# Kernel tuning notes

Measured on AMD Instinct MI355X. Metric: run time of the kernel, lower is better.

## Reference

```python
import jax, jax.numpy as jnp
import numpy as np

N_NODES = 100000


def gcn_conv(x, edge_index, edge_weight, W, b):
    """PyG GCNConv: out = D^-1/2 (A + I) D^-1/2 X W + b (self-loop weight 1)."""
    n = x.shape[0]
    src, dst = edge_index[0], edge_index[1]
    loop = jnp.arange(n)
    src_sl = jnp.concatenate([src, loop])
    dst_sl = jnp.concatenate([dst, loop])
    ew_sl = jnp.concatenate([edge_weight, jnp.ones((n,), x.dtype)])
    deg = jax.ops.segment_sum(ew_sl, dst_sl, num_segments=n)  # [N]
    dinv = jnp.where(deg > 0, jax.lax.rsqrt(deg), 0.0)
    norm = dinv[src_sl] * ew_sl * dinv[dst_sl]  # [E+N]
    h = x @ W  # [N, out_dim] dense transform before propagation
    msg = h[src_sl] * norm[:, None]  # gather + scale, [E+N, out_dim]
    out = jax.ops.segment_sum(msg, dst_sl, num_segments=n)  # scatter-add
    return out + b


def setup_inputs() -> dict:
    key = jax.random.key(0)
    ks = jax.random.split(key, 9)
    in_dim, hidden, latent = 128, 64, 32
    n, e = N_NODES, 1600000
    x = jax.random.normal(ks[0], (n, in_dim), dtype=jnp.float32)
    edge_index = jax.random.randint(ks[1], (2, e), 0, n, dtype=jnp.int64)
    edge_weight = jax.random.uniform(ks[2], (e,), dtype=jnp.float32)
    def glorot(k, fan_in, fan_out):
        s = jnp.sqrt(6.0 / (fan_in + fan_out))
        return jax.random.uniform(k, (fan_in, fan_out), jnp.float32, -s, s)
    return {
        "x": x,
        "edge_index": edge_index,
        "edge_weight": edge_weight,
        "W1": glorot(ks[3], in_dim, hidden),
        "b1": jnp.zeros((hidden,), jnp.float32),
        "W_mu": glorot(ks[4], hidden, latent),
        "b_mu": jnp.zeros((latent,), jnp.float32),
        "W_lv": glorot(ks[5], hidden, latent),
        "b_lv": jnp.zeros((latent,), jnp.float32),
    }


def reference(x, edge_index, edge_weight, W1, b1, W_mu, b_mu, W_lv, b_lv):
    h = jax.nn.relu(gcn_conv(x, edge_index, edge_weight, W1, b1))
    mu = gcn_conv(h, edge_index, edge_weight, W_mu, b_mu)
    logvar = gcn_conv(h, edge_index, edge_weight, W_lv, b_lv)
    return (mu, logvar)
```

## Files before the change

### kernel.cpp

```cpp
#include <hip/hip_runtime.h>

static __device__ __forceinline__ float4 ld4(const float* p) { return *(const float4*)p; }
static __device__ __forceinline__ float b2f(unsigned short u) {
    return __uint_as_float((unsigned)u << 16);
}
static __device__ __forceinline__ float b2f_lo(unsigned u) { return __uint_as_float(u << 16); }
static __device__ __forceinline__ float b2f_hi(unsigned u) { return __uint_as_float(u & 0xFFFF0000u); }
static __device__ __forceinline__ unsigned short f2b(float f) {
    unsigned x = __float_as_uint(f);
    return (unsigned short)((x + 0x7FFFu + ((x >> 16) & 1u)) >> 16);
}

#define NPB 512


__global__ __launch_bounds__(1024) void k_bin(const int* __restrict__ src,
                                              const int* __restrict__ dst,
                                              const float* __restrict__ ew,
                                              int* __restrict__ bin_cnt,
                                              unsigned long long* __restrict__ ebuf,
                                              int E, int capE, int NB) {
    extern __shared__ int sh[];
    int* h = sh;
    int* base = sh + NB;
    int tid = threadIdx.x;
    for (int j = tid; j < NB; j += 1024) h[j] = 0;
    __syncthreads();
    int e0 = blockIdx.x * 4096;
    unsigned long long pk[4]; int b[4], loc[4]; bool act[4];
    #pragma unroll
    for (int i = 0; i < 4; i++) {
        int e = e0 + i * 1024 + tid;
        act[i] = e < E;
        if (act[i]) {
            int s = src[e];
            int d = dst[e];
            float w = ew[e];
            b[i] = d >> 9;
            pk[i] = ((unsigned long long)__float_as_uint(w) << 32) |
                    (unsigned)((d & (NPB - 1)) << 17) | (unsigned)s;
            loc[i] = atomicAdd(&h[b[i]], 1);
        }
    }
    __syncthreads();
    for (int j = tid; j < NB; j += 1024) base[j] = atomicAdd(&bin_cnt[j], h[j]);
    __syncthreads();
    #pragma unroll
    for (int i = 0; i < 4; i++) {
        if (act[i]) ebuf[(size_t)b[i] * capE + base[b[i]] + loc[i]] = pk[i];
    }
}

__global__ __launch_bounds__(512) void k_csr_build(const unsigned long long* __restrict__ ebuf,
                                                   const int* __restrict__ bin_cnt,
                                                   int2* __restrict__ rowcnt,
                                                   float* __restrict__ dinv,
                                                   unsigned long long* __restrict__ csr,
                                                   int n, int capE) {
    __shared__ unsigned cntL[NPB];
    __shared__ unsigned ewsL[NPB];
    __shared__ int scanL[NPB];
    __shared__ int rowL[NPB];
    __shared__ unsigned fillL[NPB];
    __shared__ int binbase_s;
    int b = blockIdx.x;
    int tid = threadIdx.x;
    cntL[tid] = 0; ewsL[tid] = 0; fillL[tid] = 0;
    scanL[tid] = (tid < b) ? bin_cnt[tid] : 0;
    __syncthreads();
    int m = bin_cnt[b];
    const unsigned long long* eb = ebuf + (size_t)b * capE;
    for (int i = tid; i < m; i += 512) {
        unsigned long long pk = eb[i];
        int ld = (int)((pk >> 17) & (NPB - 1));
        float w = __uint_as_float((unsigned)(pk >> 32));
        atomicAdd(&cntL[ld], 1u);
        atomicAdd(&ewsL[ld], (unsigned)(w * 16777216.0f));
    }
    __syncthreads();
    #pragma unroll
    for (int off = 256; off > 0; off >>= 1) {
        if (tid < off) scanL[tid] += scanL[tid + off];
        __syncthreads();
    }
    if (tid == 0) binbase_s = scanL[0];
    __syncthreads();
    int v = (int)cntL[tid];
    scanL[tid] = v;
    __syncthreads();
    #pragma unroll
    for (int off = 1; off < 512; off <<= 1) {
        int t = (tid >= off) ? scanL[tid - off] : 0;
        __syncthreads();
        scanL[tid] += t;
        __syncthreads();
    }
    int rp = binbase_s + scanL[tid] - v;
    rowL[tid] = rp;
    int node = b * NPB + tid;
    if (node < n) {
        rowcnt[node] = make_int2(rp, v);
        dinv[node] = rsqrtf(1.0f + (float)ewsL[tid] * (1.0f / 16777216.0f));
    }
    __syncthreads();
    for (int i = tid; i < m; i += 512) {
        unsigned long long pk = eb[i];
        int s = (int)(pk & 0x1FFFF);
        int ld = (int)((pk >> 17) & (NPB - 1));
        int pos = rowL[ld] + (int)atomicAdd(&fillL[ld], 1u);
        csr[pos] = (unsigned long long)(unsigned)s | (pk & 0xFFFFFFFF00000000ull);
    }
}

template<int K, bool SPLITW, bool ABF16>
__global__ __launch_bounds__(256) void k_gemm(const void* __restrict__ Av,
                                              const float* __restrict__ W0,
                                              const float* __restrict__ W1s,
                                              const float* __restrict__ dinv,
                                              unsigned short* __restrict__ out, int n) {
    __shared__ float Ws[K * 64];
    __shared__ float Xs[64 * K];
    int tid = threadIdx.x;
    int row0 = blockIdx.x * 64;

    constexpr int WF4 = K * 64 / 4;
    for (int j = tid; j < WF4; j += 256) {
        float4 v;
        if (!SPLITW) {
            v = ld4(W0 + j * 4);
        } else {
            int k = (j * 4) >> 6;
            int c = (j * 4) & 63;
            v = (c < 32) ? ld4(W0 + k * 32 + c) : ld4(W1s + k * 32 + (c - 32));
        }
        *(float4*)&Ws[j * 4] = v;
    }
    constexpr int XF4PR = K / 4;
    for (int j = tid; j < 64 * XF4PR; j += 256) {
        int r = j / XF4PR, kc = j % XF4PR;
        int grow = row0 + r;
        float4 v = make_float4(0.f, 0.f, 0.f, 0.f);
        if (grow < n) {
            if (ABF16) {
                const unsigned short* Ab = (const unsigned short*)Av;
                ushort4 u = *(const ushort4*)(Ab + (size_t)grow * K + kc * 4);
                v = make_float4(b2f(u.x), b2f(u.y), b2f(u.z), b2f(u.w));
            } else {
                v = ld4((const float*)Av + (size_t)grow * K + kc * 4);
            }
        }
        *(float4*)&Xs[r * K + kc * 4] = v;
    }
    __syncthreads();

    int c0 = (tid & 15) * 4;
    int r0 = (tid >> 4) * 4;
    float4 acc[4] = {};
    #pragma unroll 4
    for (int kk = 0; kk < K; kk += 4) {
        float4 w0 = ld4(&Ws[(kk + 0) * 64 + c0]);
        float4 w1 = ld4(&Ws[(kk + 1) * 64 + c0]);
        float4 w2 = ld4(&Ws[(kk + 2) * 64 + c0]);
        float4 w3 = ld4(&Ws[(kk + 3) * 64 + c0]);
        #pragma unroll
        for (int i = 0; i < 4; i++) {
            float4 a = ld4(&Xs[(r0 + i) * K + kk]);
            acc[i].x = fmaf(a.x, w0.x, fmaf(a.y, w1.x, fmaf(a.z, w2.x, fmaf(a.w, w3.x, acc[i].x))));
            acc[i].y = fmaf(a.x, w0.y, fmaf(a.y, w1.y, fmaf(a.z, w2.y, fmaf(a.w, w3.y, acc[i].y))));
            acc[i].z = fmaf(a.x, w0.z, fmaf(a.y, w1.z, fmaf(a.z, w2.z, fmaf(a.w, w3.z, acc[i].z))));
            acc[i].w = fmaf(a.x, w0.w, fmaf(a.y, w1.w, fmaf(a.z, w2.w, fmaf(a.w, w3.w, acc[i].w))));
        }
    }
    #pragma unroll
    for (int i = 0; i < 4; i++) {
        int grow = row0 + r0 + i;
        if (grow < n) {
            float sc = dinv[grow];
            ushort4 u = make_ushort4(f2b(acc[i].x * sc), f2b(acc[i].y * sc),
                                     f2b(acc[i].z * sc), f2b(acc[i].w * sc));
            *(ushort4*)&out[(size_t)grow * 64 + c0] = u;
        }
    }
}

template<bool RELU, bool SPLIT_OUT>
__global__ __launch_bounds__(256) void k_prop(const unsigned short* __restrict__ g,
                                              const int2* __restrict__ csr,
                                              const int2* __restrict__ rowcnt,
                                              const float* __restrict__ dinv,
                                              const float* __restrict__ bias0,
                                              const float* __restrict__ bias1,
                                              void* __restrict__ outv, int n) {
    int node = blockIdx.x * 4 + (threadIdx.x >> 6);
    if (node >= n) return;
    int lane = threadIdx.x & 63;
    int q = lane >> 4;
    int t = lane & 15;
    float a0 = 0.f, a1 = 0.f, a2 = 0.f, a3 = 0.f;
    int2 rc = rowcnt[node];
    const int2* ep = csr + rc.x;
    int m = rc.y;
    for (int e = 0; e < m; e += 8) {
        int e1 = e + q, e2 = e + 4 + q;
        if (e1 < m) {
            int2 p = ep[e1];
            uint2 r = *(const uint2*)(g + (size_t)p.x * 64 + t * 4);
            float nm = __int_as_float(p.y);
            a0 = fmaf(b2f_lo(r.x), nm, a0);
            a1 = fmaf(b2f_hi(r.x), nm, a1);
            a2 = fmaf(b2f_lo(r.y), nm, a2);
            a3 = fmaf(b2f_hi(r.y), nm, a3);
        }
        if (e2 < m) {
            int2 p = ep[e2];
            uint2 r = *(const uint2*)(g + (size_t)p.x * 64 + t * 4);
            float nm = __int_as_float(p.y);
            a0 = fmaf(b2f_lo(r.x), nm, a0);
            a1 = fmaf(b2f_hi(r.x), nm, a1);
            a2 = fmaf(b2f_lo(r.y), nm, a2);
            a3 = fmaf(b2f_hi(r.y), nm, a3);
        }
    }
    a0 += __shfl_xor(a0, 16); a0 += __shfl_xor(a0, 32);
    a1 += __shfl_xor(a1, 16); a1 += __shfl_xor(a1, 32);
    a2 += __shfl_xor(a2, 16); a2 += __shfl_xor(a2, 32);
    a3 += __shfl_xor(a3, 16); a3 += __shfl_xor(a3, 32);
    if (q != 0) return;
    uint2 sr = *(const uint2*)(g + (size_t)node * 64 + t * 4);
    a0 += b2f_lo(sr.x); a1 += b2f_hi(sr.x);
    a2 += b2f_lo(sr.y); a3 += b2f_hi(sr.y);
    float di = dinv[node];
    a0 *= di; a1 *= di; a2 *= di; a3 *= di;
    if (!SPLIT_OUT) {
        float4 bb = ld4(bias0 + t * 4);
        a0 += bb.x; a1 += bb.y; a2 += bb.z; a3 += bb.w;
        if (RELU) {
            a0 = fmaxf(a0, 0.f); a1 = fmaxf(a1, 0.f);
            a2 = fmaxf(a2, 0.f); a3 = fmaxf(a3, 0.f);
        }
        ushort4 u = make_ushort4(f2b(a0), f2b(a1), f2b(a2), f2b(a3));
        *(ushort4*)((unsigned short*)outv + (size_t)node * 64 + t * 4) = u;
    } else {
        float* out = (float*)outv;
        if (t < 8) {
            float4 bb = ld4(bias0 + t * 4);
            float4 v = make_float4(a0 + bb.x, a1 + bb.y, a2 + bb.z, a3 + bb.w);
            *(float4*)&out[(size_t)node * 32 + t * 4] = v;
        } else {
            float4 bb = ld4(bias1 + (t - 8) * 4);
            float4 v = make_float4(a0 + bb.x, a1 + bb.y, a2 + bb.z, a3 + bb.w);
            *(float4*)&out[(size_t)n * 32 + (size_t)node * 32 + (t - 8) * 4] = v;
        }
    }
}

extern "C" void kernel_launch(void* const* d_in, const int* in_sizes, int n_in,
                              void* d_out, int out_size, void* d_ws, size_t ws_size,
                              hipStream_t stream) {
    const float* x   = (const float*)d_in[0];
    const int*   ei  = (const int*)d_in[1];
    const float* ew  = (const float*)d_in[2];
    const float* W1  = (const float*)d_in[3];
    const float* b1  = (const float*)d_in[4];
    const float* Wmu = (const float*)d_in[5];
    const float* bmu = (const float*)d_in[6];
    const float* Wlv = (const float*)d_in[7];
    const float* blv = (const float*)d_in[8];
    float* outp = (float*)d_out;

    const int n = in_sizes[0] / 128;
    const int E = in_sizes[2];
    const int* src = ei;
    const int* dst = ei + E;
    const int NB = (n + NPB - 1) / NPB;
    const int capE = E / NB + 2048;

    size_t o = 0;
    auto alloc = [&](size_t bytes) { void* p = (char*)d_ws + o; o += (bytes + 511) & ~(size_t)511; return p; };
    int*   bin_cnt  = (int*)alloc((size_t)NB * 4);
    int2*  rowcnt   = (int2*)alloc((size_t)n * 8);
    float* dinv     = (float*)alloc((size_t)n * 4);
    unsigned long long* csr  = (unsigned long long*)alloc((size_t)E * 8);
    unsigned long long* ebuf = (unsigned long long*)alloc((size_t)NB * capE * 8);
    unsigned short* g0 = (unsigned short*)alloc((size_t)n * 64 * 2);
    unsigned short* h  = (unsigned short*)alloc((size_t)n * 64 * 2);
    unsigned short* g2 = g0;

    hipMemsetAsync(bin_cnt, 0, (size_t)NB * 4, stream);
    k_bin<<<(E + 4095) / 4096, 1024, NB * 2 * sizeof(int), stream>>>(src, dst, ew, bin_cnt,
                                                                     ebuf, E, capE, NB);
    k_csr_build<<<NB, 512, 0, stream>>>(ebuf, bin_cnt, rowcnt, dinv, csr, n, capE);

    const int gb = (n + 63) / 64;
    k_gemm<128, false, false><<<gb, 256, 0, stream>>>(x, W1, nullptr, dinv, g0, n);
    k_prop<true, false><<<(n + 3) / 4, 256, 0, stream>>>(g0, (const int2*)csr, rowcnt, dinv,
                                                         b1, nullptr, h, n);
    k_gemm<64, true, true><<<gb, 256, 0, stream>>>(h, Wmu, Wlv, dinv, g2, n);
    k_prop<false, true><<<(n + 3) / 4, 256, 0, stream>>>(g2, (const int2*)csr, rowcnt, dinv,
                                                         bmu, blv, outp, n);
}
```

Before: 338.3 us.

## Fuse first GEMM with edge binning in one launch and stage bins in LDS

```diff
diff --git a/kernel.cpp b/kernel.cpp
--- a/kernel.cpp
+++ b/kernel.cpp
@@ -11,43 +11,94 @@
     return (unsigned short)((x + 0x7FFFu + ((x >> 16) & 1u)) >> 16);
 }
 
-#define NPB 512
-
-
-__global__ __launch_bounds__(1024) void k_bin(const int* __restrict__ src,
-                                              const int* __restrict__ dst,
-                                              const float* __restrict__ ew,
-                                              int* __restrict__ bin_cnt,
-                                              unsigned long long* __restrict__ ebuf,
-                                              int E, int capE, int NB) {
-    extern __shared__ int sh[];
-    int* h = sh;
-    int* base = sh + NB;
+#define NPB 256
+#define CAPE 5120
+
+
+__global__ __launch_bounds__(256) void k_fused1(const float* __restrict__ A,
+                                                const float* __restrict__ W0,
+                                                const float* __restrict__ dinv_unused,
+                                                unsigned short* __restrict__ gout,
+                                                const int* __restrict__ src,
+                                                const int* __restrict__ dst,
+                                                const float* __restrict__ ew,
+                                                int* __restrict__ bin_cnt,
+                                                unsigned long long* __restrict__ ebuf,
+                                                int n, int E, int gb, int NB) {
+    __shared__ float Ws[64 * 64];
+    __shared__ float Xs[64 * 64];
+    __shared__ int hist[512];
+    __shared__ int hbase[512];
     int tid = threadIdx.x;
-    for (int j = tid; j < NB; j += 1024) h[j] = 0;
-    __syncthreads();
-    int e0 = blockIdx.x * 4096;
-    unsigned long long pk[4]; int b[4], loc[4]; bool act[4];
-    #pragma unroll
-    for (int i = 0; i < 4; i++) {
-        int e = e0 + i * 1024 + tid;
-        act[i] = e < E;
-        if (act[i]) {
-            int s = src[e];
-            int d = dst[e];
-            float w = ew[e];
-            b[i] = d >> 9;
-            pk[i] = ((unsigned long long)__float_as_uint(w) << 32) |
-                    (unsigned)((d & (NPB - 1)) << 17) | (unsigned)s;
-            loc[i] = atomicAdd(&h[b[i]], 1);
-        }
-    }
-    __syncthreads();
-    for (int j = tid; j < NB; j += 1024) base[j] = atomicAdd(&bin_cnt[j], h[j]);
-    __syncthreads();
-    #pragma unroll
-    for (int i = 0; i < 4; i++) {
-        if (act[i]) ebuf[(size_t)b[i] * capE + base[b[i]] + loc[i]] = pk[i];
+
+    if ((int)blockIdx.x < gb) {
+        int row0 = blockIdx.x * 64;
+        int c0 = (tid & 15) * 4;
+        int r0 = (tid >> 4) * 4;
+        float4 acc[4] = {};
+        #pragma unroll
+        for (int p = 0; p < 2; p++) {
+            for (int j = tid; j < 1024; j += 256)
+                *(float4*)&Ws[j * 4] = ld4(W0 + p * 4096 + j * 4);
+            for (int j = tid; j < 1024; j += 256) {
+                int r = j >> 4, kc = j & 15;
+                int grow = row0 + r;
+                float4 v = make_float4(0.f, 0.f, 0.f, 0.f);
+                if (grow < n) v = ld4(A + (size_t)grow * 128 + p * 64 + kc * 4);
+                *(float4*)&Xs[r * 64 + kc * 4] = v;
+            }
+            __syncthreads();
+            #pragma unroll 4
+            for (int kk = 0; kk < 64; kk += 4) {
+                float4 w0 = ld4(&Ws[(kk + 0) * 64 + c0]);
+                float4 w1 = ld4(&Ws[(kk + 1) * 64 + c0]);
+                float4 w2 = ld4(&Ws[(kk + 2) * 64 + c0]);
+                float4 w3 = ld4(&Ws[(kk + 3) * 64 + c0]);
+                #pragma unroll
+                for (int i = 0; i < 4; i++) {
+                    float4 a = ld4(&Xs[(r0 + i) * 64 + kk]);
+                    acc[i].x = fmaf(a.x, w0.x, fmaf(a.y, w1.x, fmaf(a.z, w2.x, fmaf(a.w, w3.x, acc[i].x))));
+                    acc[i].y = fmaf(a.x, w0.y, fmaf(a.y, w1.y, fmaf(a.z, w2.y, fmaf(a.w, w3.y, acc[i].y))));
+                    acc[i].z = fmaf(a.x, w0.z, fmaf(a.y, w1.z, fmaf(a.z, w2.z, fmaf(a.w, w3.z, acc[i].z))));
+                    acc[i].w = fmaf(a.x, w0.w, fmaf(a.y, w1.w, fmaf(a.z, w2.w, fmaf(a.w, w3.w, acc[i].w))));
+                }
+            }
+            __syncthreads();
+        }
+        #pragma unroll
+        for (int i = 0; i < 4; i++) {
+            int grow = row0 + r0 + i;
+            if (grow < n) {
+                ushort4 u = make_ushort4(f2b(acc[i].x), f2b(acc[i].y), f2b(acc[i].z), f2b(acc[i].w));
+                *(ushort4*)&gout[(size_t)grow * 64 + c0] = u;
+            }
+        }
+    } else {
+        for (int j = tid; j < NB; j += 256) hist[j] = 0;
+        __syncthreads();
+        int e0 = ((int)blockIdx.x - gb) * 4096;
+        unsigned long long pk[16]; int bb[16]; int loc[16];
+        #pragma unroll
+        for (int j = 0; j < 16; j++) {
+            int e = e0 + j * 256 + tid;
+            if (e < E) {
+                int s = src[e];
+                int d = dst[e];
+                float w = ew[e];
+                bb[j] = d >> 8;
+                pk[j] = ((unsigned long long)__float_as_uint(w) << 32) |
+                        (unsigned)((d & (NPB - 1)) << 17) | (unsigned)s;
+                loc[j] = atomicAdd(&hist[bb[j]], 1);
+            } else bb[j] = -1;
+        }
+        __syncthreads();
+        for (int j = tid; j < NB; j += 256) hbase[j] = atomicAdd(&bin_cnt[j], hist[j]);
+        __syncthreads();
+        #pragma unroll
+        for (int j = 0; j < 16; j++) {
+            if (bb[j] >= 0)
+                ebuf[(size_t)bb[j] * CAPE + hbase[bb[j]] + loc[j]] = pk[j];
+        }
     }
 }
 
@@ -56,22 +107,24 @@
                                                    int2* __restrict__ rowcnt,
                                                    float* __restrict__ dinv,
                                                    unsigned long long* __restrict__ csr,
-                                                   int n, int capE) {
+                                                   int n) {
+    __shared__ unsigned long long eL[CAPE];
     __shared__ unsigned cntL[NPB];
     __shared__ unsigned ewsL[NPB];
-    __shared__ int scanL[NPB];
+    __shared__ unsigned fillL[NPB];
+    __shared__ int scanL[512];
     __shared__ int rowL[NPB];
-    __shared__ unsigned fillL[NPB];
     __shared__ int binbase_s;
     int b = blockIdx.x;
     int tid = threadIdx.x;
-    cntL[tid] = 0; ewsL[tid] = 0; fillL[tid] = 0;
+    if (tid < NPB) { cntL[tid] = 0; ewsL[tid] = 0; fillL[tid] = 0; }
     scanL[tid] = (tid < b) ? bin_cnt[tid] : 0;
     __syncthreads();
     int m = bin_cnt[b];
-    const unsigned long long* eb = ebuf + (size_t)b * capE;
+    const unsigned long long* eb = ebuf + (size_t)b * CAPE;
     for (int i = tid; i < m; i += 512) {
         unsigned long long pk = eb[i];
+        eL[i] = pk;
         int ld = (int)((pk >> 17) & (NPB - 1));
         float w = __uint_as_float((unsigned)(pk >> 32));
         atomicAdd(&cntL[ld], 1u);
@@ -85,7 +138,7 @@
     }
     if (tid == 0) binbase_s = scanL[0];
     __syncthreads();
-    int v = (int)cntL[tid];
+    int v = (tid < NPB) ? (int)cntL[tid] : 0;
     scanL[tid] = v;
     __syncthreads();
     #pragma unroll
@@ -95,21 +148,35 @@
         scanL[tid] += t;
         __syncthreads();
     }
-    int rp = binbase_s + scanL[tid] - v;
-    rowL[tid] = rp;
-    int node = b * NPB + tid;
-    if (node < n) {
-        rowcnt[node] = make_int2(rp, v);
-        dinv[node] = rsqrtf(1.0f + (float)ewsL[tid] * (1.0f / 16777216.0f));
+    if (tid < NPB) {
+        int rp = binbase_s + scanL[tid] - v;
+        rowL[tid] = rp;
+        int node = b * NPB + tid;
+        if (node < n) {
+            rowcnt[node] = make_int2(rp, v);
+            dinv[node] = rsqrtf(1.0f + (float)ewsL[tid] * (1.0f / 16777216.0f));
+        }
     }
     __syncthreads();
     for (int i = tid; i < m; i += 512) {
-        unsigned long long pk = eb[i];
+        unsigned long long pk = eL[i];
         int s = (int)(pk & 0x1FFFF);
         int ld = (int)((pk >> 17) & (NPB - 1));
         int pos = rowL[ld] + (int)atomicAdd(&fillL[ld], 1u);
         csr[pos] = (unsigned long long)(unsigned)s | (pk & 0xFFFFFFFF00000000ull);
     }
+}
+
+__global__ __launch_bounds__(256) void k_scale(unsigned short* __restrict__ h0,
+                                               const float* __restrict__ dinv, int n) {
+    int i = blockIdx.x * 256 + threadIdx.x;
+    if (i >= n * 16) return;
+    int node = i >> 4;
+    float sc = dinv[node];
+    ushort4 u = *(ushort4*)&h0[(size_t)i * 4];
+    u = make_ushort4(f2b(b2f(u.x) * sc), f2b(b2f(u.y) * sc),
+                     f2b(b2f(u.z) * sc), f2b(b2f(u.w) * sc));
+    *(ushort4*)&h0[(size_t)i * 4] = u;
 }
 
 template<int K, bool SPLITW, bool ABF16>
@@ -273,7 +340,6 @@
     const int* src = ei;
     const int* dst = ei + E;
     const int NB = (n + NPB - 1) / NPB;
-    const int capE = E / NB + 2048;
 
     size_t o = 0;
     auto alloc = [&](size_t bytes) { void* p = (char*)d_ws + o; o += (bytes + 511) & ~(size_t)511; return p; };
@@ -281,18 +347,19 @@
     int2*  rowcnt   = (int2*)alloc((size_t)n * 8);
     float* dinv     = (float*)alloc((size_t)n * 4);
     unsigned long long* csr  = (unsigned long long*)alloc((size_t)E * 8);
-    unsigned long long* ebuf = (unsigned long long*)alloc((size_t)NB * capE * 8);
+    unsigned long long* ebuf = (unsigned long long*)alloc((size_t)NB * CAPE * 8);
     unsigned short* g0 = (unsigned short*)alloc((size_t)n * 64 * 2);
     unsigned short* h  = (unsigned short*)alloc((size_t)n * 64 * 2);
     unsigned short* g2 = g0;
 
+    const int gb = (n + 63) / 64;
+    const int bb = (E + 4095) / 4096;
+
     hipMemsetAsync(bin_cnt, 0, (size_t)NB * 4, stream);
-    k_bin<<<(E + 4095) / 4096, 1024, NB * 2 * sizeof(int), stream>>>(src, dst, ew, bin_cnt,
-                                                                     ebuf, E, capE, NB);
-    k_csr_build<<<NB, 512, 0, stream>>>(ebuf, bin_cnt, rowcnt, dinv, csr, n, capE);
-
-    const int gb = (n + 63) / 64;
-    k_gemm<128, false, false><<<gb, 256, 0, stream>>>(x, W1, nullptr, dinv, g0, n);
+    k_fused1<<<gb + bb, 256, 0, stream>>>(x, W1, nullptr, g0, src, dst, ew,
+                                          bin_cnt, ebuf, n, E, gb, NB);
+    k_csr_build<<<NB, 512, 0, stream>>>(ebuf, bin_cnt, rowcnt, dinv, csr, n);
+    k_scale<<<(n * 16 + 255) / 256, 256, 0, stream>>>(g0, dinv, n);
     k_prop<true, false><<<(n + 3) / 4, 256, 0, stream>>>(g0, (const int2*)csr, rowcnt, dinv,
                                                          b1, nullptr, h, n);
     k_gemm<64, true, true><<<gb, 256, 0, stream>>>(h, Wmu, Wlv, dinv, g2, n);
```

Result: faster. 319.0 us (-5.7%).
